# Kernel tuning notes

Measured on AMD Instinct MI355X. Metric: run time of the kernel, lower is better.

Reference implementation:

```python
import jax, jax.numpy as jnp
import numpy as np

B, S, DIM = 2, 2048, 2048
NH, NKV, HD = 32, 8, 64
N_REP = NH // NKV


def apply_rope(x, cos, sin):
    # x: (B, H, S, HD); cos/sin: (S, HD//2)
    d = x.shape[-1] // 2
    x1, x2 = x[..., :d], x[..., d:]
    c = cos[None, None, :, :]
    s = sin[None, None, :, :]
    return jnp.concatenate([x1 * c - x2 * s, x2 * c + x1 * s], axis=-1)


def setup_inputs() -> dict:
    key = jax.random.key(0)
    ks = jax.random.split(key, 8)
    x = jax.random.normal(ks[0], (B, S, DIM), dtype=jnp.float32)
    # plausible RoPE tables
    inv_freq = 1.0 / (10000.0 ** (jnp.arange(0, HD, 2, dtype=jnp.float32) / HD))
    t = jnp.arange(S, dtype=jnp.float32)
    freqs = jnp.outer(t, inv_freq)  # (S, HD//2)
    rope_cos = jnp.cos(freqs)
    rope_sin = jnp.sin(freqs)
    doc_ids = jnp.sort(jax.random.randint(ks[1], (B, S), 0, 8, dtype=jnp.int32), axis=-1)
    std = 0.02
    Wq = jax.random.normal(ks[2], (NH * HD, DIM), dtype=jnp.float32) * std
    Wk = jax.random.normal(ks[3], (NKV * HD, DIM), dtype=jnp.float32) * std
    Wv = jax.random.normal(ks[4], (NKV * HD, DIM), dtype=jnp.float32) * std
    Wo = jax.random.normal(ks[5], (DIM, NH * HD), dtype=jnp.float32) * std
    return {"x": x, "rope_cos": rope_cos, "rope_sin": rope_sin,
            "doc_ids": doc_ids, "Wq": Wq, "Wk": Wk, "Wv": Wv, "Wo": Wo}


def reference(x, rope_cos, rope_sin, doc_ids, Wq, Wk, Wv, Wo):
    batch, seq_len, _ = x.shape
    q = (x @ Wq.T).reshape(batch, seq_len, NH, HD).transpose(0, 2, 1, 3)   # (B,NH,S,HD)
    k = (x @ Wk.T).reshape(batch, seq_len, NKV, HD).transpose(0, 2, 1, 3)  # (B,NKV,S,HD)
    v = (x @ Wv.T).reshape(batch, seq_len, NKV, HD).transpose(0, 2, 1, 3)

    q = apply_rope(q, rope_cos, rope_sin)
    k = apply_rope(k, rope_cos, rope_sin)

    # GQA expansion (repeat_interleave on head dim)
    k = jnp.repeat(k, N_REP, axis=1)  # (B,NH,S,HD)
    v = jnp.repeat(v, N_REP, axis=1)

    # block-diagonal causal mask from packed doc ids
    doc_mask = doc_ids[:, :, None] == doc_ids[:, None, :]          # (B,S,S)
    causal = jnp.tril(jnp.ones((seq_len, seq_len), dtype=bool))    # (S,S)
    mask = (doc_mask & causal[None])[:, None, :, :]                # (B,1,S,S)

    scale = 1.0 / jnp.sqrt(jnp.asarray(HD, dtype=q.dtype))
    scores = jnp.einsum("bhqd,bhkd->bhqk", q, k) * scale
    scores = jnp.where(mask, scores, jnp.finfo(scores.dtype).min)
    attn = jax.nn.softmax(scores, axis=-1)
    out = jnp.einsum("bhqk,bhkd->bhqd", attn, v)                   # (B,NH,S,HD)
    out = out.transpose(0, 2, 1, 3).reshape(batch, seq_len, NH * HD)
    return out @ Wo.T
```

## Files before the change

### kernel.cpp

```cpp
#include <hip/hip_runtime.h>
#include <hip/hip_bf16.h>

#define BB   2
#define SEQ  2048
#define DIMD 2048
#define NHH  32
#define NKVV 8
#define HDD  64
#define QKVS 3072

typedef __bf16 bf16x8 __attribute__((ext_vector_type(8)));
typedef float  floatx4 __attribute__((ext_vector_type(4)));

typedef __attribute__((address_space(1))) const void* gas_ptr;
typedef __attribute__((address_space(3))) void*       las_ptr;

#define MFMA16 __builtin_amdgcn_mfma_f32_16x16x32_bf16
#define CBAR() asm volatile("" ::: "memory")

__device__ __forceinline__ unsigned short f2bu(float f) {
    __hip_bfloat16 h = __float2bfloat16(f);
    return *reinterpret_cast<unsigned short*>(&h);
}

#define C_X  (8u  * 1024 * 1024)
#define C_WQ (4u  * 1024 * 1024)
#define C_WK (1u  * 1024 * 1024)
#define C_WV (1u  * 1024 * 1024)
#define C_WO (4u  * 1024 * 1024)
__global__ void cvt_all(const float* __restrict__ x,  const float* __restrict__ wq,
                        const float* __restrict__ wk, const float* __restrict__ wv,
                        const float* __restrict__ wo,
                        __hip_bfloat16* __restrict__ xb,
                        __hip_bfloat16* __restrict__ wqkv,
                        __hip_bfloat16* __restrict__ wob)
{
    unsigned i = (blockIdx.x * blockDim.x + threadIdx.x) * 4;
    const float* src; __hip_bfloat16* dst;
    if (i < C_X)                       { src = x  + i;                    dst = xb + i; }
    else if (i < C_X + C_WQ)           { unsigned o = i - C_X;            src = wq + o; dst = wqkv + o; }
    else if (i < C_X + C_WQ + C_WK)    { unsigned o = i - C_X - C_WQ;     src = wk + o; dst = wqkv + C_WQ + o; }
    else if (i < C_X + C_WQ + C_WK + C_WV) { unsigned o = i - C_X - C_WQ - C_WK; src = wv + o; dst = wqkv + C_WQ + C_WK + o; }
    else                               { unsigned o = i - C_X - C_WQ - C_WK - C_WV; if (o >= C_WO) return; src = wo + o; dst = wob + o; }
    float4 v = *reinterpret_cast<const float4*>(src);
    dst[0] = __float2bfloat16(v.x);
    dst[1] = __float2bfloat16(v.y);
    dst[2] = __float2bfloat16(v.z);
    dst[3] = __float2bfloat16(v.w);
}

template <typename OutT, bool ROPE, int BN>
__global__ __launch_bounds__(512, 2) void gemm8p(
    const __hip_bfloat16* __restrict__ Abf,
    const __hip_bfloat16* __restrict__ Wbf,
    OutT* __restrict__ C,
    int M, int N, int K, int ldc,
    const float* __restrict__ cosb, const float* __restrict__ sinb)
{
    constexpr int  NF = BN / 64;
    constexpr int  WN = BN / 4;
    constexpr bool B2 = (BN == 256);
    constexpr int  HB = (BN / 2) * 64;

    const __bf16* Ag = reinterpret_cast<const __bf16*>(Abf);
    const __bf16* Wg = reinterpret_cast<const __bf16*>(Wbf);

    __shared__ __align__(16) __bf16 As[2][256 * 64];
    __shared__ __align__(16) __bf16 Bs[2][BN * 64];

    const int NT   = K >> 6;
    const int tid  = threadIdx.x;
    const int wid  = tid >> 6;
    const int lane = tid & 63;
    const int l15  = lane & 15;
    const int l4   = lane >> 4;
    const int wm   = wid >> 2;
    const int wn   = wid & 3;

    const int gx   = M >> 8;
    const int nwg  = (int)gridDim.x;
    const int orig = (int)blockIdx.x;
    const int wg   = (orig & 7) * (nwg >> 3) + (orig >> 3);
    const int bm   = (wg % gx) << 8;
    const int bn   = (wg / gx) * BN;

    const int r0 = tid >> 3;
    const int c0 = ((tid & 7) ^ (r0 & 7)) * 8;
    const __bf16* aS00 = Ag + (size_t)(bm + r0) * K + c0;
    const __bf16* aS01 = aS00 + (size_t)64  * K;
    const __bf16* aS10 = aS00 + (size_t)128 * K;
    const __bf16* aS11 = aS00 + (size_t)192 * K;
    const __bf16* bS00 = Wg + (size_t)(bn + r0) * K + c0;
    const __bf16* bS01 = bS00 + (size_t)64 * K;
    const __bf16* bS10 = bS00 + (size_t)(BN / 2) * K;
    const __bf16* bS11 = bS10 + (size_t)64 * K;

    bf16x8 af[4][2], b01[2][2], b23[2][2];
    floatx4 acc[8][NF] = {};

    auto stage2 = [&](const __bf16* s0, const __bf16* s1, __bf16* d, int kt) {
        int k0 = (kt < NT ? kt : NT - 1) << 6;
        __builtin_amdgcn_global_load_lds((gas_ptr)(s0 + k0), (las_ptr)(d + tid * 8), 16, 0, 0);
        if (s1)
        __builtin_amdgcn_global_load_lds((gas_ptr)(s1 + k0), (las_ptr)(d + 4096 + tid * 8), 16, 0, 0);
    };
    auto lda = [&](int buf, int mbase) {
        #pragma unroll
        for (int mi = 0; mi < 4; ++mi)
            #pragma unroll
            for (int kk = 0; kk < 2; ++kk) {
                int row = wm * 128 + (mbase + mi) * 16 + l15;
                int ch  = ((kk * 4 + l4) ^ (row & 7)) * 8;
                af[mi][kk] = *reinterpret_cast<const bf16x8*>(&As[buf][row * 64 + ch]);
            }
    };
    auto ldb = [&](int buf, bf16x8 (&regs)[2][2], int nbase) {
        #pragma unroll
        for (int ni = 0; ni < 2; ++ni)
            #pragma unroll
            for (int kk = 0; kk < 2; ++kk) {
                int row = wn * WN + (nbase + ni) * 16 + l15;
                int ch  = ((kk * 4 + l4) ^ (row & 7)) * 8;
                regs[ni][kk] = *reinterpret_cast<const bf16x8*>(&Bs[buf][row * 64 + ch]);
            }
    };
    auto mmBoth = [&](int mbase, bf16x8 (&bregs)[2][2], int nb) {
        #pragma unroll
        for (int mi = 0; mi < 4; ++mi)
            #pragma unroll
            for (int ni = 0; ni < 2; ++ni) {
                acc[mbase + mi][nb + ni] = MFMA16(af[mi][0], bregs[ni][0], acc[mbase + mi][nb + ni], 0, 0, 0);
                acc[mbase + mi][nb + ni] = MFMA16(af[mi][1], bregs[ni][1], acc[mbase + mi][nb + ni], 0, 0, 0);
            }
    };
    auto mmOne = [&](int mbase, int kk) {
        #pragma unroll
        for (int mi = 0; mi < 4; ++mi)
            #pragma unroll
            for (int ni = 0; ni < 2; ++ni)
                acc[mbase + mi][ni] = MFMA16(af[mi][kk], b01[ni][kk], acc[mbase + mi][ni], 0, 0, 0);
    };

    auto ktile = [&](int cur, int t) {
        lda(cur, 0);
        ldb(cur, b01, 0);
        stage2(aS10, aS11, &As[cur ^ 1][8192], t + 1);
        CBAR(); __builtin_amdgcn_s_barrier(); CBAR();
        asm volatile("s_waitcnt lgkmcnt(0)" ::: "memory");
        __builtin_amdgcn_sched_barrier(0);
        __builtin_amdgcn_s_setprio(1);
        if constexpr (B2) mmBoth(0, b01, 0); else mmOne(0, 0);
        __builtin_amdgcn_s_setprio(0);
        CBAR(); __builtin_amdgcn_s_barrier(); CBAR();
        if constexpr (B2) ldb(cur, b23, 2);
        stage2(bS00, B2 ? bS01 : (const __bf16*)nullptr, &Bs[cur ^ 1][0], t + 1);
        CBAR(); __builtin_amdgcn_s_barrier(); CBAR();
        asm volatile("s_waitcnt lgkmcnt(0)" ::: "memory");
        __builtin_amdgcn_sched_barrier(0);
        __builtin_amdgcn_s_setprio(1);
        if constexpr (B2) mmBoth(0, b23, 2); else mmOne(0, 1);
        __builtin_amdgcn_s_setprio(0);
        CBAR(); __builtin_amdgcn_s_barrier(); CBAR();
        lda(cur, 4);
        stage2(bS10, B2 ? bS11 : (const __bf16*)nullptr, &Bs[cur ^ 1][HB], t + 1);
        CBAR(); __builtin_amdgcn_s_barrier(); CBAR();
        asm volatile("s_waitcnt lgkmcnt(0)" ::: "memory");
        __builtin_amdgcn_sched_barrier(0);
        __builtin_amdgcn_s_setprio(1);
        if constexpr (B2) mmBoth(4, b23, 2); else mmOne(4, 1);
        __builtin_amdgcn_s_setprio(0);
        CBAR(); __builtin_amdgcn_s_barrier(); CBAR();
        stage2(aS00, aS01, &As[cur][0], t + 2);
        CBAR(); __builtin_amdgcn_s_barrier(); CBAR();
        __builtin_amdgcn_s_setprio(1);
        if constexpr (B2) mmBoth(4, b01, 0); else mmOne(4, 0);
        __builtin_amdgcn_s_setprio(0);
        asm volatile("s_waitcnt vmcnt(2)" ::: "memory");
        CBAR(); __builtin_amdgcn_s_barrier(); CBAR();
    };

    stage2(aS00, aS01, &As[0][0],    0);
    stage2(aS10, aS11, &As[0][8192], 0);
    stage2(bS00, B2 ? bS01 : (const __bf16*)nullptr, &Bs[0][0],  0);
    stage2(bS10, B2 ? bS11 : (const __bf16*)nullptr, &Bs[0][HB], 0);
    stage2(aS00, aS01, &As[1][0],    1);
    asm volatile("s_waitcnt vmcnt(2)" ::: "memory");
    CBAR(); __builtin_amdgcn_s_barrier(); CBAR();

    #pragma unroll 1
    for (int t = 0; t < NT; t += 2) {
        ktile(0, t);
        ktile(1, t + 1);
    }

    if constexpr (ROPE) {
        bool do_rope = (bn + wn * 64) < 2560;
        #pragma unroll
        for (int mi = 0; mi < 8; ++mi) {
            #pragma unroll
            for (int r = 0; r < 4; ++r) {
                int row = bm + wm * 128 + mi * 16 + l4 * 4 + r;
                int s   = row & (SEQ - 1);
                #pragma unroll
                for (int j = 0; j < 2; ++j) {
                    float x1 = acc[mi][j][r], x2 = acc[mi][j + 2][r];
                    if (do_rope) {
                        float cf = cosb[s * 32 + j * 16 + l15];
                        float sf = sinb[s * 32 + j * 16 + l15];
                        float o1 = x1 * cf - x2 * sf;
                        float o2 = x2 * cf + x1 * sf;
                        x1 = o1; x2 = o2;
                    }
                    int col = bn + wn * 64 + j * 16 + l15;
                    C[(size_t)row * ldc + col]      = __float2bfloat16(x1);
                    C[(size_t)row * ldc + col + 32] = __float2bfloat16(x2);
                }
            }
        }
    } else {
        #pragma unroll
        for (int mi = 0; mi < 8; ++mi)
            #pragma unroll
            for (int ni = 0; ni < NF; ++ni)
                #pragma unroll
                for (int r = 0; r < 4; ++r) {
                    int row = bm + wm * 128 + mi * 16 + l4 * 4 + r;
                    int col = bn + wn * WN + ni * 16 + l15;
                    if constexpr (sizeof(OutT) == 4)
                        C[(size_t)row * ldc + col] = acc[mi][ni][r];
                    else
                        C[(size_t)row * ldc + col] = __float2bfloat16(acc[mi][ni][r]);
                }
    }
}

__global__ void transpose_v(const __hip_bfloat16* __restrict__ qkv,
                            unsigned short* __restrict__ vT)
{
    __shared__ unsigned short T[64][68];
    int s0  = blockIdx.x * 64;
    int kvh = blockIdx.y;
    int b   = blockIdx.z;
    int tid = threadIdx.x;

    int srow = tid >> 2, dg = (tid & 3) * 16;
    const unsigned short* src = reinterpret_cast<const unsigned short*>(qkv)
        + (size_t)(b * SEQ + s0 + srow) * QKVS + 2560 + kvh * 64 + dg;
    #pragma unroll
    for (int i = 0; i < 4; ++i)
        *reinterpret_cast<ushort4*>(&T[srow][dg + i * 4]) =
            *reinterpret_cast<const ushort4*>(src + i * 4);
    __syncthreads();

    int drow = tid >> 2, sg = (tid & 3) * 16;
    unsigned short* dst = vT + ((size_t)(b * NKVV + kvh) * 64 + drow) * SEQ + s0 + sg;
    #pragma unroll
    for (int i = 0; i < 4; ++i) {
        ushort4 u;
        u.x = T[sg + i * 4 + 0][drow];
        u.y = T[sg + i * 4 + 1][drow];
        u.z = T[sg + i * 4 + 2][drow];
        u.w = T[sg + i * 4 + 3][drow];
        *reinterpret_cast<ushort4*>(dst + i * 4) = u;
    }
}

__global__ __launch_bounds__(256) void attn_mfma(
    const __hip_bfloat16* __restrict__ qkv,
    const unsigned short* __restrict__ vT,
    const int* __restrict__ doc,
    __hip_bfloat16* __restrict__ ob)
{
    int qblk = (int)gridDim.x - 1 - (int)blockIdx.x;
    int h    = blockIdx.y;
    int b    = blockIdx.z;
    int kvh  = h >> 2;
    int tid  = threadIdx.x;
    int wv   = tid >> 6;
    int lane = tid & 63;
    int l15  = lane & 15;
    int l4   = lane >> 4;
    int q0   = qblk * 128;
    int qw   = q0 + wv * 32;

    __shared__ unsigned short Ks[64 * 64];
    __shared__ unsigned short Vts[64 * 64];
    __shared__ unsigned short Pb[4][32][76];
    __shared__ int kdoc[64];

    const unsigned short* qus = reinterpret_cast<const unsigned short*>(qkv);
    const unsigned short* kus = qus + 2048;

    bf16x8 aq[2][2];
    #pragma unroll
    for (int qt = 0; qt < 2; ++qt) {
        const unsigned short* qrow = qus + (size_t)(b * SEQ + qw + qt * 16 + l15) * QKVS + h * HDD;
        aq[qt][0] = *reinterpret_cast<const bf16x8*>(qrow + l4 * 8);
        aq[qt][1] = *reinterpret_cast<const bf16x8*>(qrow + 32 + l4 * 8);
    }
    int qd[2][4];
    #pragma unroll
    for (int qt = 0; qt < 2; ++qt)
        #pragma unroll
        for (int r = 0; r < 4; ++r)
            qd[qt][r] = doc[b * SEQ + qw + qt * 16 + l4 * 4 + r];
    int qd_w   = doc[b * SEQ + qw];
    int qd_blk = doc[b * SEQ + q0];

    float mrow[2][4], lrow[2][4];
    #pragma unroll
    for (int qt = 0; qt < 2; ++qt)
        #pragma unroll
        for (int r = 0; r < 4; ++r) { mrow[qt][r] = -1e30f; lrow[qt][r] = 0.f; }
    floatx4 accO[2][4] = {};

    int slot0 = tid, slot1 = tid + 256;
    int row0 = slot0 >> 3, g0 = (slot0 & 7) ^ (row0 & 7);
    int row1 = slot1 >> 3, g1 = (slot1 & 7) ^ (row1 & 7);
    const unsigned short* vtb = vT + ((size_t)(b * NKVV + kvh) * 64) * SEQ;

    int kc_end = 2 * qblk + 1;
    for (int kc = 0; kc <= kc_end; ++kc) {
        int k0 = kc * 64;
        int kd_last = doc[b * SEQ + k0 + 63];
        if (kd_last < qd_blk) continue;

        __syncthreads();
        __builtin_amdgcn_global_load_lds(
            (gas_ptr)(kus + (size_t)(b * SEQ + k0 + row0) * QKVS + kvh * HDD + g0 * 8),
            (las_ptr)(Ks + slot0 * 8), 16, 0, 0);
        __builtin_amdgcn_global_load_lds(
            (gas_ptr)(kus + (size_t)(b * SEQ + k0 + row1) * QKVS + kvh * HDD + g1 * 8),
            (las_ptr)(Ks + slot1 * 8), 16, 0, 0);
        __builtin_amdgcn_global_load_lds(
            (gas_ptr)(vtb + (size_t)row0 * SEQ + k0 + g0 * 8),
            (las_ptr)(Vts + slot0 * 8), 16, 0, 0);
        __builtin_amdgcn_global_load_lds(
            (gas_ptr)(vtb + (size_t)row1 * SEQ + k0 + g1 * 8),
            (las_ptr)(Vts + slot1 * 8), 16, 0, 0);
        if (tid < 64) kdoc[tid] = doc[b * SEQ + k0 + tid];
        __syncthreads();

        if (k0 <= qw + 31 && kd_last >= qd_w) {
            #pragma unroll
            for (int qt = 0; qt < 2; ++qt) {
                float s[4][4];
                #pragma unroll
                for (int t = 0; t < 4; ++t) {
                    int krow = t * 16 + l15;
                    bf16x8 bk0 = *reinterpret_cast<const bf16x8*>(Ks + krow * 64 + ((l4 ^ (krow & 7)) * 8));
                    bf16x8 bk1 = *reinterpret_cast<const bf16x8*>(Ks + krow * 64 + ((((l4 + 4)) ^ (krow & 7)) * 8));
                    floatx4 acc = {};
                    acc = MFMA16(aq[qt][0], bk0, acc, 0, 0, 0);
                    acc = MFMA16(aq[qt][1], bk1, acc, 0, 0, 0);
                    int key = k0 + krow;
                    int kd  = kdoc[krow];
                    #pragma unroll
                    for (int r = 0; r < 4; ++r) {
                        int qrow = qw + qt * 16 + l4 * 4 + r;
                        bool valid = (kd == qd[qt][r]) && (key <= qrow);
                        s[t][r] = valid ? acc[r] * 0.125f : -1e30f;
                    }
                }
                #pragma unroll
                for (int r = 0; r < 4; ++r) {
                    float pm = fmaxf(fmaxf(s[0][r], s[1][r]), fmaxf(s[2][r], s[3][r]));
                    pm = fmaxf(pm, __shfl_xor(pm, 1));
                    pm = fmaxf(pm, __shfl_xor(pm, 2));
                    pm = fmaxf(pm, __shfl_xor(pm, 4));
                    pm = fmaxf(pm, __shfl_xor(pm, 8));
                    float mnew = fmaxf(mrow[qt][r], pm);
                    float alpha = __expf(mrow[qt][r] - mnew);
                    mrow[qt][r] = mnew;
                    float ps = 0.f;
                    #pragma unroll
                    for (int t = 0; t < 4; ++t) {
                        float p = (s[t][r] <= -1e29f) ? 0.f : __expf(s[t][r] - mnew);
                        Pb[wv][qt * 16 + l4 * 4 + r][t * 16 + l15] = f2bu(p);
                        ps += p;
                    }
                    ps += __shfl_xor(ps, 1);
                    ps += __shfl_xor(ps, 2);
                    ps += __shfl_xor(ps, 4);
                    ps += __shfl_xor(ps, 8);
                    lrow[qt][r] = lrow[qt][r] * alpha + ps;
                    #pragma unroll
                    for (int t = 0; t < 4; ++t) accO[qt][t][r] *= alpha;
                }
            }
            #pragma unroll
            for (int qt = 0; qt < 2; ++qt) {
                bf16x8 ap0 = *reinterpret_cast<const bf16x8*>(&Pb[wv][qt * 16 + l15][l4 * 8]);
                bf16x8 ap1 = *reinterpret_cast<const bf16x8*>(&Pb[wv][qt * 16 + l15][32 + l4 * 8]);
                #pragma unroll
                for (int t = 0; t < 4; ++t) {
                    int vrow = t * 16 + l15;
                    bf16x8 bv0 = *reinterpret_cast<const bf16x8*>(Vts + vrow * 64 + ((l4 ^ (vrow & 7)) * 8));
                    bf16x8 bv1 = *reinterpret_cast<const bf16x8*>(Vts + vrow * 64 + ((((l4 + 4)) ^ (vrow & 7)) * 8));
                    accO[qt][t] = MFMA16(ap0, bv0, accO[qt][t], 0, 0, 0);
                    accO[qt][t] = MFMA16(ap1, bv1, accO[qt][t], 0, 0, 0);
                }
            }
        }
    }

    #pragma unroll
    for (int qt = 0; qt < 2; ++qt)
        #pragma unroll
        for (int r = 0; r < 4; ++r) {
            float inv = 1.0f / lrow[qt][r];
            size_t base = (size_t)(b * SEQ + qw + qt * 16 + l4 * 4 + r) * (NHH * HDD) + h * HDD;
            #pragma unroll
            for (int t = 0; t < 4; ++t)
                ob[base + t * 16 + l15] = __float2bfloat16(accO[qt][t][r] * inv);
        }
}

extern "C" void kernel_launch(void* const* d_in, const int* in_sizes, int n_in,
                              void* d_out, int out_size, void* d_ws, size_t ws_size,
                              hipStream_t stream) {
    const float* x  = (const float*)d_in[0];
    const float* rc = (const float*)d_in[1];
    const float* rs = (const float*)d_in[2];
    const int*   dc = (const int*)d_in[3];
    const float* Wq = (const float*)d_in[4];
    const float* Wk = (const float*)d_in[5];
    const float* Wv = (const float*)d_in[6];
    const float* Wo = (const float*)d_in[7];
    float* out = (float*)d_out;

    const int M    = BB * SEQ;
    const int KVD  = NKVV * HDD;
    const int QKVN = DIMD + 2 * KVD;

    char* ws = (char*)d_ws;
    size_t off = 0;
    auto alloc = [&](size_t elems) { __hip_bfloat16* p = (__hip_bfloat16*)(ws + off); off += elems * 2; return p; };
    __hip_bfloat16* xb   = alloc((size_t)M * DIMD);
    __hip_bfloat16* wqkv = alloc((size_t)QKVN * DIMD);
    __hip_bfloat16* wob  = alloc((size_t)DIMD * DIMD);
    __hip_bfloat16* qkv  = alloc((size_t)M * QKVN);
    __hip_bfloat16* abuf = alloc((size_t)M * DIMD);
    unsigned short* vtb  = (unsigned short*)alloc((size_t)BB * NKVV * HDD * SEQ);

    {
        unsigned total4 = (C_X + C_WQ + C_WK + C_WV + C_WO) / 4;
        cvt_all<<<dim3((total4 + 255) / 256), 256, 0, stream>>>(
            x, Wq, Wk, Wv, Wo, xb, wqkv, wob);
    }

    gemm8p<__hip_bfloat16, true, 256><<<dim3((M / 256) * (QKVN / 256)), 512, 0, stream>>>(
        xb, wqkv, qkv, M, QKVN, DIMD, QKVN, rc, rs);

    transpose_v<<<dim3(SEQ / 64, NKVV, BB), 256, 0, stream>>>(qkv, vtb);

    attn_mfma<<<dim3(SEQ / 128, NHH, BB), 256, 0, stream>>>(qkv, vtb, dc, abuf);

    gemm8p<float, false, 128><<<dim3((M / 256) * (DIMD / 128)), 512, 0, stream>>>(
        abuf, wob, out, M, DIMD, DIMD, DIMD, nullptr, nullptr);
}
```

Measured before the change: 298.3 us.

## Replace 8-phase 256-tile GEMM with simple 128x128 double-buffered GEMM and fuse V transpose

Replaces the heavily pipelined 512-thread 256xBN GEMM with a simpler 256-thread 128x128 tile kernel that uses one stage per k-tile and full vmcnt waits. The QKV GEMM epilogue now writes V directly in transposed layout, which removes the separate transpose_v kernel launch and its round trip through memory. The aim is more workgroups for better occupancy and load balance, plus one fewer kernel. The cost is losing the fine-grained load/compute interleaving and halving per-tile reuse, and the transposed V stores are strided and uncoalesced.

```diff
diff --git a/kernel.cpp b/kernel.cpp
--- a/kernel.cpp
+++ b/kernel.cpp
@@ -49,24 +49,20 @@
     dst[3] = __float2bfloat16(v.w);
 }
 
-template <typename OutT, bool ROPE, int BN>
-__global__ __launch_bounds__(512, 2) void gemm8p(
+template <typename OutT, bool ROPE>
+__global__ __launch_bounds__(256, 2) void gemm2p(
     const __hip_bfloat16* __restrict__ Abf,
     const __hip_bfloat16* __restrict__ Wbf,
     OutT* __restrict__ C,
     int M, int N, int K, int ldc,
-    const float* __restrict__ cosb, const float* __restrict__ sinb)
+    const float* __restrict__ cosb, const float* __restrict__ sinb,
+    unsigned short* __restrict__ vT)
 {
-    constexpr int  NF = BN / 64;
-    constexpr int  WN = BN / 4;
-    constexpr bool B2 = (BN == 256);
-    constexpr int  HB = (BN / 2) * 64;
-
     const __bf16* Ag = reinterpret_cast<const __bf16*>(Abf);
     const __bf16* Wg = reinterpret_cast<const __bf16*>(Wbf);
 
-    __shared__ __align__(16) __bf16 As[2][256 * 64];
-    __shared__ __align__(16) __bf16 Bs[2][BN * 64];
+    __shared__ __align__(16) __bf16 As[2][128 * 64];
+    __shared__ __align__(16) __bf16 Bs[2][128 * 64];
 
     const int NT   = K >> 6;
     const int tid  = threadIdx.x;
@@ -74,194 +70,134 @@
     const int lane = tid & 63;
     const int l15  = lane & 15;
     const int l4   = lane >> 4;
-    const int wm   = wid >> 2;
-    const int wn   = wid & 3;
-
-    const int gx   = M >> 8;
+    const int wm   = wid >> 1;
+    const int wn   = wid & 1;
+
+    const int gx   = M >> 7;
     const int nwg  = (int)gridDim.x;
     const int orig = (int)blockIdx.x;
     const int wg   = (orig & 7) * (nwg >> 3) + (orig >> 3);
-    const int bm   = (wg % gx) << 8;
-    const int bn   = (wg / gx) * BN;
-
-    const int r0 = tid >> 3;
-    const int c0 = ((tid & 7) ^ (r0 & 7)) * 8;
-    const __bf16* aS00 = Ag + (size_t)(bm + r0) * K + c0;
-    const __bf16* aS01 = aS00 + (size_t)64  * K;
-    const __bf16* aS10 = aS00 + (size_t)128 * K;
-    const __bf16* aS11 = aS00 + (size_t)192 * K;
-    const __bf16* bS00 = Wg + (size_t)(bn + r0) * K + c0;
-    const __bf16* bS01 = bS00 + (size_t)64 * K;
-    const __bf16* bS10 = bS00 + (size_t)(BN / 2) * K;
-    const __bf16* bS11 = bS10 + (size_t)64 * K;
-
-    bf16x8 af[4][2], b01[2][2], b23[2][2];
-    floatx4 acc[8][NF] = {};
-
-    auto stage2 = [&](const __bf16* s0, const __bf16* s1, __bf16* d, int kt) {
-        int k0 = (kt < NT ? kt : NT - 1) << 6;
-        __builtin_amdgcn_global_load_lds((gas_ptr)(s0 + k0), (las_ptr)(d + tid * 8), 16, 0, 0);
-        if (s1)
-        __builtin_amdgcn_global_load_lds((gas_ptr)(s1 + k0), (las_ptr)(d + 4096 + tid * 8), 16, 0, 0);
+    const int bm   = (wg % gx) << 7;
+    const int bn   = (wg / gx) << 7;
+
+    const __bf16* aSrc[4];
+    const __bf16* bSrc[4];
+    #pragma unroll
+    for (int i = 0; i < 4; ++i) {
+        int slot = tid + 256 * i;
+        int r = slot >> 3;
+        int c = ((slot & 7) ^ (r & 7)) * 8;
+        aSrc[i] = Ag + (size_t)(bm + r) * K + c;
+        bSrc[i] = Wg + (size_t)(bn + r) * K + c;
+    }
+
+    auto stage = [&](int buf, int kt) {
+        int k0 = (kt < NT ? kt : 0) << 6;
+        #pragma unroll
+        for (int i = 0; i < 4; ++i)
+            __builtin_amdgcn_global_load_lds((gas_ptr)(aSrc[i] + k0),
+                (las_ptr)(&As[buf][(tid + 256 * i) * 8]), 16, 0, 0);
+        #pragma unroll
+        for (int i = 0; i < 4; ++i)
+            __builtin_amdgcn_global_load_lds((gas_ptr)(bSrc[i] + k0),
+                (las_ptr)(&Bs[buf][(tid + 256 * i) * 8]), 16, 0, 0);
     };
-    auto lda = [&](int buf, int mbase) {
+
+    bf16x8 af[4][2], bfr[4][2];
+    floatx4 acc[4][4] = {};
+
+    stage(0, 0);
+    asm volatile("s_waitcnt vmcnt(0)" ::: "memory");
+    CBAR(); __builtin_amdgcn_s_barrier(); CBAR();
+
+    int cur = 0;
+    #pragma unroll 1
+    for (int t = 0; t < NT; ++t) {
+        stage(cur ^ 1, t + 1);
         #pragma unroll
         for (int mi = 0; mi < 4; ++mi)
             #pragma unroll
             for (int kk = 0; kk < 2; ++kk) {
-                int row = wm * 128 + (mbase + mi) * 16 + l15;
+                int row = wm * 64 + mi * 16 + l15;
                 int ch  = ((kk * 4 + l4) ^ (row & 7)) * 8;
-                af[mi][kk] = *reinterpret_cast<const bf16x8*>(&As[buf][row * 64 + ch]);
-            }
-    };
-    auto ldb = [&](int buf, bf16x8 (&regs)[2][2], int nbase) {
-        #pragma unroll
-        for (int ni = 0; ni < 2; ++ni)
+                af[mi][kk] = *reinterpret_cast<const bf16x8*>(&As[cur][row * 64 + ch]);
+            }
+        #pragma unroll
+        for (int ni = 0; ni < 4; ++ni)
             #pragma unroll
             for (int kk = 0; kk < 2; ++kk) {
-                int row = wn * WN + (nbase + ni) * 16 + l15;
+                int row = wn * 64 + ni * 16 + l15;
                 int ch  = ((kk * 4 + l4) ^ (row & 7)) * 8;
-                regs[ni][kk] = *reinterpret_cast<const bf16x8*>(&Bs[buf][row * 64 + ch]);
-            }
-    };
-    auto mmBoth = [&](int mbase, bf16x8 (&bregs)[2][2], int nb) {
-        #pragma unroll
-        for (int mi = 0; mi < 4; ++mi)
-            #pragma unroll
-            for (int ni = 0; ni < 2; ++ni) {
-                acc[mbase + mi][nb + ni] = MFMA16(af[mi][0], bregs[ni][0], acc[mbase + mi][nb + ni], 0, 0, 0);
-                acc[mbase + mi][nb + ni] = MFMA16(af[mi][1], bregs[ni][1], acc[mbase + mi][nb + ni], 0, 0, 0);
-            }
-    };
-    auto mmOne = [&](int mbase, int kk) {
-        #pragma unroll
-        for (int mi = 0; mi < 4; ++mi)
-            #pragma unroll
-            for (int ni = 0; ni < 2; ++ni)
-                acc[mbase + mi][ni] = MFMA16(af[mi][kk], b01[ni][kk], acc[mbase + mi][ni], 0, 0, 0);
-    };
-
-    auto ktile = [&](int cur, int t) {
-        lda(cur, 0);
-        ldb(cur, b01, 0);
-        stage2(aS10, aS11, &As[cur ^ 1][8192], t + 1);
-        CBAR(); __builtin_amdgcn_s_barrier(); CBAR();
+                bfr[ni][kk] = *reinterpret_cast<const bf16x8*>(&Bs[cur][row * 64 + ch]);
+            }
         asm volatile("s_waitcnt lgkmcnt(0)" ::: "memory");
         __builtin_amdgcn_sched_barrier(0);
         __builtin_amdgcn_s_setprio(1);
-        if constexpr (B2) mmBoth(0, b01, 0); else mmOne(0, 0);
+        #pragma unroll
+        for (int mi = 0; mi < 4; ++mi)
+            #pragma unroll
+            for (int ni = 0; ni < 4; ++ni) {
+                acc[mi][ni] = MFMA16(af[mi][0], bfr[ni][0], acc[mi][ni], 0, 0, 0);
+                acc[mi][ni] = MFMA16(af[mi][1], bfr[ni][1], acc[mi][ni], 0, 0, 0);
+            }
         __builtin_amdgcn_s_setprio(0);
+        asm volatile("s_waitcnt vmcnt(0)" ::: "memory");
         CBAR(); __builtin_amdgcn_s_barrier(); CBAR();
-        if constexpr (B2) ldb(cur, b23, 2);
-        stage2(bS00, B2 ? bS01 : (const __bf16*)nullptr, &Bs[cur ^ 1][0], t + 1);
-        CBAR(); __builtin_amdgcn_s_barrier(); CBAR();
-        asm volatile("s_waitcnt lgkmcnt(0)" ::: "memory");
-        __builtin_amdgcn_sched_barrier(0);
-        __builtin_amdgcn_s_setprio(1);
-        if constexpr (B2) mmBoth(0, b23, 2); else mmOne(0, 1);
-        __builtin_amdgcn_s_setprio(0);
-        CBAR(); __builtin_amdgcn_s_barrier(); CBAR();
-        lda(cur, 4);
-        stage2(bS10, B2 ? bS11 : (const __bf16*)nullptr, &Bs[cur ^ 1][HB], t + 1);
-        CBAR(); __builtin_amdgcn_s_barrier(); CBAR();
-        asm volatile("s_waitcnt lgkmcnt(0)" ::: "memory");
-        __builtin_amdgcn_sched_barrier(0);
-        __builtin_amdgcn_s_setprio(1);
-        if constexpr (B2) mmBoth(4, b23, 2); else mmOne(4, 1);
-        __builtin_amdgcn_s_setprio(0);
-        CBAR(); __builtin_amdgcn_s_barrier(); CBAR();
-        stage2(aS00, aS01, &As[cur][0], t + 2);
-        CBAR(); __builtin_amdgcn_s_barrier(); CBAR();
-        __builtin_amdgcn_s_setprio(1);
-        if constexpr (B2) mmBoth(4, b01, 0); else mmOne(4, 0);
-        __builtin_amdgcn_s_setprio(0);
-        asm volatile("s_waitcnt vmcnt(2)" ::: "memory");
-        CBAR(); __builtin_amdgcn_s_barrier(); CBAR();
-    };
-
-    stage2(aS00, aS01, &As[0][0],    0);
-    stage2(aS10, aS11, &As[0][8192], 0);
-    stage2(bS00, B2 ? bS01 : (const __bf16*)nullptr, &Bs[0][0],  0);
-    stage2(bS10, B2 ? bS11 : (const __bf16*)nullptr, &Bs[0][HB], 0);
-    stage2(aS00, aS01, &As[1][0],    1);
-    asm volatile("s_waitcnt vmcnt(2)" ::: "memory");
-    CBAR(); __builtin_amdgcn_s_barrier(); CBAR();
-
-    #pragma unroll 1
-    for (int t = 0; t < NT; t += 2) {
-        ktile(0, t);
-        ktile(1, t + 1);
-    }
-
+        cur ^= 1;
+    }
+
+    const int col0 = bn + wn * 64;
     if constexpr (ROPE) {
-        bool do_rope = (bn + wn * 64) < 2560;
-        #pragma unroll
-        for (int mi = 0; mi < 8; ++mi) {
-            #pragma unroll
-            for (int r = 0; r < 4; ++r) {
-                int row = bm + wm * 128 + mi * 16 + l4 * 4 + r;
-                int s   = row & (SEQ - 1);
-                #pragma unroll
-                for (int j = 0; j < 2; ++j) {
-                    float x1 = acc[mi][j][r], x2 = acc[mi][j + 2][r];
-                    if (do_rope) {
+        if (col0 >= 2560) {
+            int kvh = (col0 - 2560) >> 6;
+            #pragma unroll
+            for (int mi = 0; mi < 4; ++mi)
+                #pragma unroll
+                for (int r = 0; r < 4; ++r) {
+                    int row = bm + wm * 64 + mi * 16 + l4 * 4 + r;
+                    int b = row >> 11, s = row & (SEQ - 1);
+                    #pragma unroll
+                    for (int ni = 0; ni < 4; ++ni) {
+                        int d = ni * 16 + l15;
+                        vT[((size_t)(b * NKVV + kvh) * 64 + d) * SEQ + s] =
+                            f2bu(acc[mi][ni][r]);
+                    }
+                }
+        } else {
+            #pragma unroll
+            for (int mi = 0; mi < 4; ++mi) {
+                #pragma unroll
+                for (int r = 0; r < 4; ++r) {
+                    int row = bm + wm * 64 + mi * 16 + l4 * 4 + r;
+                    int s   = row & (SEQ - 1);
+                    #pragma unroll
+                    for (int j = 0; j < 2; ++j) {
+                        float x1 = acc[mi][j][r], x2 = acc[mi][j + 2][r];
                         float cf = cosb[s * 32 + j * 16 + l15];
                         float sf = sinb[s * 32 + j * 16 + l15];
                         float o1 = x1 * cf - x2 * sf;
                         float o2 = x2 * cf + x1 * sf;
-                        x1 = o1; x2 = o2;
+                        int col = col0 + j * 16 + l15;
+                        C[(size_t)row * ldc + col]      = __float2bfloat16(o1);
+                        C[(size_t)row * ldc + col + 32] = __float2bfloat16(o2);
                     }
-                    int col = bn + wn * 64 + j * 16 + l15;
-                    C[(size_t)row * ldc + col]      = __float2bfloat16(x1);
-                    C[(size_t)row * ldc + col + 32] = __float2bfloat16(x2);
                 }
             }
         }
     } else {
         #pragma unroll
-        for (int mi = 0; mi < 8; ++mi)
-            #pragma unroll
-            for (int ni = 0; ni < NF; ++ni)
+        for (int mi = 0; mi < 4; ++mi)
+            #pragma unroll
+            for (int ni = 0; ni < 4; ++ni)
                 #pragma unroll
                 for (int r = 0; r < 4; ++r) {
-                    int row = bm + wm * 128 + mi * 16 + l4 * 4 + r;
-                    int col = bn + wn * WN + ni * 16 + l15;
+                    int row = bm + wm * 64 + mi * 16 + l4 * 4 + r;
+                    int col = col0 + ni * 16 + l15;
                     if constexpr (sizeof(OutT) == 4)
                         C[(size_t)row * ldc + col] = acc[mi][ni][r];
                     else
                         C[(size_t)row * ldc + col] = __float2bfloat16(acc[mi][ni][r]);
                 }
-    }
-}
-
-__global__ void transpose_v(const __hip_bfloat16* __restrict__ qkv,
-                            unsigned short* __restrict__ vT)
-{
-    __shared__ unsigned short T[64][68];
-    int s0  = blockIdx.x * 64;
-    int kvh = blockIdx.y;
-    int b   = blockIdx.z;
-    int tid = threadIdx.x;
-
-    int srow = tid >> 2, dg = (tid & 3) * 16;
-    const unsigned short* src = reinterpret_cast<const unsigned short*>(qkv)
-        + (size_t)(b * SEQ + s0 + srow) * QKVS + 2560 + kvh * 64 + dg;
-    #pragma unroll
-    for (int i = 0; i < 4; ++i)
-        *reinterpret_cast<ushort4*>(&T[srow][dg + i * 4]) =
-            *reinterpret_cast<const ushort4*>(src + i * 4);
-    __syncthreads();
-
-    int drow = tid >> 2, sg = (tid & 3) * 16;
-    unsigned short* dst = vT + ((size_t)(b * NKVV + kvh) * 64 + drow) * SEQ + s0 + sg;
-    #pragma unroll
-    for (int i = 0; i < 4; ++i) {
-        ushort4 u;
-        u.x = T[sg + i * 4 + 0][drow];
-        u.y = T[sg + i * 4 + 1][drow];
-        u.z = T[sg + i * 4 + 2][drow];
-        u.w = T[sg + i * 4 + 3][drow];
-        *reinterpret_cast<ushort4*>(dst + i * 4) = u;
     }
 }
 
@@ -449,13 +385,11 @@
             x, Wq, Wk, Wv, Wo, xb, wqkv, wob);
     }
 
-    gemm8p<__hip_bfloat16, true, 256><<<dim3((M / 256) * (QKVN / 256)), 512, 0, stream>>>(
-        xb, wqkv, qkv, M, QKVN, DIMD, QKVN, rc, rs);
-
-    transpose_v<<<dim3(SEQ / 64, NKVV, BB), 256, 0, stream>>>(qkv, vtb);
+    gemm2p<__hip_bfloat16, true><<<dim3((M / 128) * (QKVN / 128)), 256, 0, stream>>>(
+        xb, wqkv, qkv, M, QKVN, DIMD, QKVN, rc, rs, vtb);
 
     attn_mfma<<<dim3(SEQ / 128, NHH, BB), 256, 0, stream>>>(qkv, vtb, dc, abuf);
 
-    gemm8p<float, false, 128><<<dim3((M / 256) * (DIMD / 128)), 512, 0, stream>>>(
-        abuf, wob, out, M, DIMD, DIMD, DIMD, nullptr, nullptr);
-}
+    gemm2p<float, false><<<dim3((M / 128) * (DIMD / 128)), 256, 0, stream>>>(
+        abuf, wob, out, M, DIMD, DIMD, DIMD, nullptr, nullptr, nullptr);
+}
```

Measured after the change: 301.3 us. Within noise of the previous version (+1.0%).
